# Optimization experiments

Measured on AMD Instinct MI355X. Metric: run time of the kernel, lower is better.

Reference implementation:

```python
import jax, jax.numpy as jnp
import numpy as np


def setup_inputs() -> dict:
    key = jax.random.key(0)
    k1, k2, k3, k4 = jax.random.split(key, 4)
    B, n, f, k = 32768, 512, 30, 40
    X = jax.random.normal(k1, (B, n), dtype=jnp.float32)
    w1 = jax.random.normal(k2, (n, 1), dtype=jnp.float32) * 0.01
    b = jnp.zeros((1,), dtype=jnp.float32)
    v = jax.random.normal(k3, (n, f, k), dtype=jnp.float32) * 0.01
    feature2field = jax.random.randint(k4, (n,), 0, f, dtype=jnp.int32)
    return {"X": X, "w1": w1, "b": b, "v": v, "feature2field": feature2field}


def reference(X, w1, b, v, feature2field):
    # linear terms: [B]
    linear = (X @ w1).reshape(-1) + b[0]
    n = v.shape[0]
    # A[i, j] = v[i, feature2field[j]]  -> [n, n, k]
    A = v[:, feature2field, :]
    # pair coefficient C[i, j] = sum_k v[i, field[j], k] * v[j, field[i], k]
    C = jnp.einsum('ijk,jik->ij', A, A)
    # strict upper triangle matches the i<j loop in the original
    Cm = C * jnp.triu(jnp.ones((n, n), dtype=C.dtype), k=1)
    # interaction[b] = sum_{i<j} C[i,j] * X[b,i] * X[b,j]
    inter = jnp.einsum('bi,ij,bj->b', X, Cm, X)
    logits = linear + inter
    return jax.nn.sigmoid(logits)
```

## Files before the change

kernel.cpp:

```cpp
#include <hip/hip_runtime.h>
#include <hip/hip_bf16.h>
#include <math.h>


#define N_FEAT 512
#define FK 1200
#define KDIM 40
#define B_ROWS 32768
#define BM 64
#define BK 64

typedef __attribute__((ext_vector_type(8))) short short8;
typedef __attribute__((ext_vector_type(4))) float f32x4;

__device__ __forceinline__ unsigned short bf16_rne(float f) {
    union { float f; unsigned int u; } c; c.f = f;
    unsigned int u = c.u;
    u += 0x7fffu + ((u >> 16) & 1u);
    return (unsigned short)(u >> 16);
}

__device__ __forceinline__ float bf16_to_f(unsigned short h) {
    union { unsigned int u; float f; } c;
    c.u = ((unsigned int)h) << 16;
    return c.f;
}

__device__ __forceinline__ void async_copy16(const void* g, void* l) {
    __builtin_amdgcn_global_load_lds(
        (const __attribute__((address_space(1))) void*)g,
        (__attribute__((address_space(3))) void*)l,
        16, 0, 0);
}

__global__ __launch_bounds__(256) void build_w16(const float* __restrict__ v,
                                                 const int* __restrict__ f2f,
                                                 unsigned short* __restrict__ W16) {
    const int j = blockIdx.x * 256 + threadIdx.x;
    const int i = blockIdx.y;
    const int fi = f2f[i];
    const int fj = f2f[j];
    const float4* a = (const float4*)(v + (size_t)i * FK + (size_t)fj * KDIM);
    const float4* c = (const float4*)(v + (size_t)j * FK + (size_t)fi * KDIM);
    float acc = 0.f;
#pragma unroll
    for (int q = 0; q < KDIM / 4; ++q) {
        float4 av = a[q], cv = c[q];
        acc = fmaf(av.x, cv.x, acc);
        acc = fmaf(av.y, cv.y, acc);
        acc = fmaf(av.z, cv.z, acc);
        acc = fmaf(av.w, cv.w, acc);
    }
    W16[(size_t)i * N_FEAT + j] = (i == j) ? (unsigned short)0 : bf16_rne(0.5f * acc);
}

__global__ __launch_bounds__(256, 2) void ffm_fused(const float* __restrict__ X,
                                                    const unsigned short* __restrict__ W16,
                                                    const float* __restrict__ w1,
                                                    const float* __restrict__ bvec,
                                                    float* __restrict__ out) {
    __shared__ __align__(16) unsigned short As[BM * N_FEAT];
    __shared__ __align__(16) unsigned short Bs[128 * BK];
    float* part = (float*)Bs;

    const int tid  = threadIdx.x;
    const int lane = tid & 63;
    const int wave = tid >> 6;
    const int wm = wave & 1;
    const int wn = wave >> 1;
    const int quad = lane >> 4;
    const int l16  = lane & 15;

    const size_t row0 = (size_t)blockIdx.x * BM;

    {
        const float4* X4 = (const float4*)(X + row0 * N_FEAT);
        for (int u = 0; u < 16; ++u) {
            const int g  = u * 256 + tid;
            const int r  = g >> 6;
            const int cc = g & 63;
            float4 f0 = X4[r * 128 + cc * 2];
            float4 f1 = X4[r * 128 + cc * 2 + 1];
            union { unsigned short us[8]; short8 v; } pk;
            pk.us[0] = bf16_rne(f0.x);
            pk.us[1] = bf16_rne(f0.y);
            pk.us[2] = bf16_rne(f0.z);
            pk.us[3] = bf16_rne(f0.w);
            pk.us[4] = bf16_rne(f1.x);
            pk.us[5] = bf16_rne(f1.y);
            pk.us[6] = bf16_rne(f1.z);
            pk.us[7] = bf16_rne(f1.w);
            *(short8*)(As + r * N_FEAT + ((cc ^ (r & 7)) << 3)) = pk.v;
        }
    }

    const int srow = lane >> 3;
    const int scol = (((lane & 7) ^ srow) << 3);
    const int aswz = l16 & 7;

    float rs[2][4];
#pragma unroll
    for (int mi = 0; mi < 2; ++mi)
#pragma unroll
        for (int reg = 0; reg < 4; ++reg) rs[mi][reg] = 0.f;

    for (int cb = 0; cb < 4; ++cb) {
        const int col0 = cb * 128;

        f32x4 acc[2][4];
#pragma unroll
        for (int mi = 0; mi < 2; ++mi)
#pragma unroll
            for (int ni = 0; ni < 4; ++ni)
                acc[mi][ni] = (f32x4){0.f, 0.f, 0.f, 0.f};

        for (int k0 = 0; k0 < N_FEAT; k0 += BK) {
            __syncthreads();
#pragma unroll
            for (int c = 0; c < 4; ++c) {
                const int chunk = wave * 4 + c;
                const int r = chunk * 8 + srow;
                async_copy16(W16 + (size_t)(col0 + r) * N_FEAT + k0 + scol,
                             Bs + chunk * 512);
            }
            __syncthreads();

#pragma unroll
            for (int kk = 0; kk < 2; ++kk) {
                short8 a[2], b[4];
                const int kc = (k0 >> 3) + kk * 4 + quad;
#pragma unroll
                for (int mi = 0; mi < 2; ++mi) {
                    const int ar = wm * 32 + mi * 16 + l16;
                    a[mi] = *(const short8*)(As + ar * N_FEAT + ((kc ^ aswz) << 3));
                }
                const int swc = ((kk * 4 + quad) ^ aswz) << 3;
#pragma unroll
                for (int ni = 0; ni < 4; ++ni) {
                    const int br = wn * 64 + ni * 16 + l16;
                    b[ni] = *(const short8*)(Bs + br * BK + swc);
                }
#pragma unroll
                for (int mi = 0; mi < 2; ++mi)
#pragma unroll
                    for (int ni = 0; ni < 4; ++ni)
                        acc[mi][ni] = __builtin_amdgcn_mfma_f32_16x16x32_bf16(
                            a[mi], b[ni], acc[mi][ni], 0, 0, 0);
            }
        }

        float w1v[4];
#pragma unroll
        for (int ni = 0; ni < 4; ++ni)
            w1v[ni] = w1[col0 + wn * 64 + ni * 16 + l16];
#pragma unroll
        for (int mi = 0; mi < 2; ++mi) {
#pragma unroll
            for (int ni = 0; ni < 4; ++ni) {
                const int gc = col0 + wn * 64 + ni * 16 + l16;
#pragma unroll
                for (int reg = 0; reg < 4; ++reg) {
                    const int row = wm * 32 + mi * 16 + quad * 4 + reg;
                    const int adr = row * N_FEAT + ((((gc >> 3) ^ (row & 7)) << 3) | (gc & 7));
                    const float xf = bf16_to_f(As[adr]);
                    rs[mi][reg] = fmaf(xf, acc[mi][ni][reg] + w1v[ni], rs[mi][reg]);
                }
            }
        }
    }

    __syncthreads();

#pragma unroll
    for (int mi = 0; mi < 2; ++mi)
#pragma unroll
        for (int reg = 0; reg < 4; ++reg) {
            float r = rs[mi][reg];
#pragma unroll
            for (int off = 1; off < 16; off <<= 1)
                r += __shfl_xor(r, off, 16);
            if (l16 == 0)
                part[wn * BM + wm * 32 + mi * 16 + quad * 4 + reg] = r;
        }
    __syncthreads();

    if (tid < BM) {
        const float t = part[tid] + part[BM + tid] + bvec[0];
        out[row0 + tid] = 1.0f / (1.0f + expf(-t));
    }
}

extern "C" void kernel_launch(void* const* d_in, const int* in_sizes, int n_in,
                              void* d_out, int out_size, void* d_ws, size_t ws_size,
                              hipStream_t stream) {
    const float* X   = (const float*)d_in[0];
    const float* w1  = (const float*)d_in[1];
    const float* b   = (const float*)d_in[2];
    const float* v   = (const float*)d_in[3];
    const int*   f2f = (const int*)d_in[4];
    float* out = (float*)d_out;

    unsigned short* W16 = (unsigned short*)d_ws;

    build_w16<<<dim3(2, N_FEAT), 256, 0, stream>>>(v, f2f, W16);
    ffm_fused<<<B_ROWS / BM, 256, 0, stream>>>(X, W16, w1, b, out);
}
```

Before: 126.3 us.

## Pipeline W tile loads with 4-stage LDS ring and compute linear term in fp32

Replaces the synchronous load-then-compute loop over W tiles with a flattened 32-step schedule that prefetches two tiles ahead into a 4-buffer LDS ring. It uses vmcnt waits plus one barrier per step instead of two __syncthreads. The linear term is now computed in fp32 during X staging via a wave reduction, rather than being added to the accumulators in the epilogue. LDS use grows to about 128KB and launch bounds drop to one block per CU, so occupancy falls in exchange for overlapping global-to-LDS copies with MFMA work.

```diff
diff --git a/kernel.cpp b/kernel.cpp
--- a/kernel.cpp
+++ b/kernel.cpp
@@ -8,7 +8,6 @@
 #define KDIM 40
 #define B_ROWS 32768
 #define BM 64
-#define BK 64
 
 typedef __attribute__((ext_vector_type(8))) short short8;
 typedef __attribute__((ext_vector_type(4))) float f32x4;
@@ -54,14 +53,15 @@
     W16[(size_t)i * N_FEAT + j] = (i == j) ? (unsigned short)0 : bf16_rne(0.5f * acc);
 }
 
-__global__ __launch_bounds__(256, 2) void ffm_fused(const float* __restrict__ X,
+__global__ __launch_bounds__(256, 1) void ffm_fused(const float* __restrict__ X,
                                                     const unsigned short* __restrict__ W16,
                                                     const float* __restrict__ w1,
                                                     const float* __restrict__ bvec,
                                                     float* __restrict__ out) {
     __shared__ __align__(16) unsigned short As[BM * N_FEAT];
-    __shared__ __align__(16) unsigned short Bs[128 * BK];
-    float* part = (float*)Bs;
+    __shared__ __align__(16) unsigned short Bs[4][128 * 64];
+    __shared__ float part[2][BM];
+    __shared__ float plin[BM];
 
     const int tid  = threadIdx.x;
     const int lane = tid & 63;
@@ -70,15 +70,18 @@
     const int wn = wave >> 1;
     const int quad = lane >> 4;
     const int l16  = lane & 15;
+    const int aswz = l16 & 7;
 
     const size_t row0 = (size_t)blockIdx.x * BM;
 
     {
         const float4* X4 = (const float4*)(X + row0 * N_FEAT);
+        const float4 wA = ((const float4*)w1)[lane * 2];
+        const float4 wB = ((const float4*)w1)[lane * 2 + 1];
+#pragma unroll
         for (int u = 0; u < 16; ++u) {
-            const int g  = u * 256 + tid;
-            const int r  = g >> 6;
-            const int cc = g & 63;
+            const int r  = u * 4 + wave;
+            const int cc = lane;
             float4 f0 = X4[r * 128 + cc * 2];
             float4 f1 = X4[r * 128 + cc * 2 + 1];
             union { unsigned short us[8]; short8 v; } pk;
@@ -91,85 +94,108 @@
             pk.us[6] = bf16_rne(f1.z);
             pk.us[7] = bf16_rne(f1.w);
             *(short8*)(As + r * N_FEAT + ((cc ^ (r & 7)) << 3)) = pk.v;
-        }
-    }
+            float lp = f0.x * wA.x + f0.y * wA.y + f0.z * wA.z + f0.w * wA.w
+                     + f1.x * wB.x + f1.y * wB.y + f1.z * wB.z + f1.w * wB.w;
+#pragma unroll
+            for (int off = 1; off < 64; off <<= 1)
+                lp += __shfl_xor(lp, off, 64);
+            if (lane == 0) plin[r] = lp;
+        }
+    }
+    __syncthreads();
 
     const int srow = lane >> 3;
-    const int scol = (((lane & 7) ^ srow) << 3);
-    const int aswz = l16 & 7;
+    const int scol = ((lane & 7) ^ srow) << 3;
 
     float rs[2][4];
+    f32x4 acc[2][4];
 #pragma unroll
     for (int mi = 0; mi < 2; ++mi)
 #pragma unroll
+        for (int ni = 0; ni < 4; ++ni) {
+            acc[mi][ni] = (f32x4){0.f, 0.f, 0.f, 0.f};
+            if (ni < 4) {}
+        }
+#pragma unroll
+    for (int mi = 0; mi < 2; ++mi)
+#pragma unroll
         for (int reg = 0; reg < 4; ++reg) rs[mi][reg] = 0.f;
 
-    for (int cb = 0; cb < 4; ++cb) {
-        const int col0 = cb * 128;
-
-        f32x4 acc[2][4];
-#pragma unroll
-        for (int mi = 0; mi < 2; ++mi)
-#pragma unroll
-            for (int ni = 0; ni < 4; ++ni)
-                acc[mi][ni] = (f32x4){0.f, 0.f, 0.f, 0.f};
-
-        for (int k0 = 0; k0 < N_FEAT; k0 += BK) {
-            __syncthreads();
-#pragma unroll
-            for (int c = 0; c < 4; ++c) {
-                const int chunk = wave * 4 + c;
-                const int r = chunk * 8 + srow;
-                async_copy16(W16 + (size_t)(col0 + r) * N_FEAT + k0 + scol,
-                             Bs + chunk * 512);
+    auto stage = [&](int t) {
+        unsigned short* buf = &Bs[t & 3][0];
+        const int col0 = (t >> 3) * 128;
+        const int k0   = (t & 7) * 64;
+#pragma unroll
+        for (int c = 0; c < 4; ++c) {
+            const int chunk = wave * 4 + c;
+            const int r = chunk * 8 + srow;
+            async_copy16(W16 + (size_t)(col0 + r) * N_FEAT + k0 + scol,
+                         buf + chunk * 512);
+        }
+    };
+
+    auto compute = [&](int t) {
+        const unsigned short* buf = &Bs[t & 3][0];
+        const int k0 = (t & 7) * 64;
+#pragma unroll
+        for (int kk = 0; kk < 2; ++kk) {
+            short8 a[2], b[4];
+            const int kc = (k0 >> 3) + kk * 4 + quad;
+#pragma unroll
+            for (int mi = 0; mi < 2; ++mi) {
+                const int ar = wm * 32 + mi * 16 + l16;
+                a[mi] = *(const short8*)(As + ar * N_FEAT + ((kc ^ aswz) << 3));
             }
-            __syncthreads();
-
-#pragma unroll
-            for (int kk = 0; kk < 2; ++kk) {
-                short8 a[2], b[4];
-                const int kc = (k0 >> 3) + kk * 4 + quad;
-#pragma unroll
-                for (int mi = 0; mi < 2; ++mi) {
-                    const int ar = wm * 32 + mi * 16 + l16;
-                    a[mi] = *(const short8*)(As + ar * N_FEAT + ((kc ^ aswz) << 3));
-                }
-                const int swc = ((kk * 4 + quad) ^ aswz) << 3;
-#pragma unroll
-                for (int ni = 0; ni < 4; ++ni) {
-                    const int br = wn * 64 + ni * 16 + l16;
-                    b[ni] = *(const short8*)(Bs + br * BK + swc);
-                }
-#pragma unroll
-                for (int mi = 0; mi < 2; ++mi)
-#pragma unroll
-                    for (int ni = 0; ni < 4; ++ni)
-                        acc[mi][ni] = __builtin_amdgcn_mfma_f32_16x16x32_bf16(
-                            a[mi], b[ni], acc[mi][ni], 0, 0, 0);
+            const int swc = ((kk * 4 + quad) ^ aswz) << 3;
+#pragma unroll
+            for (int ni = 0; ni < 4; ++ni) {
+                const int br = wn * 64 + ni * 16 + l16;
+                b[ni] = *(const short8*)(buf + br * 64 + swc);
             }
-        }
-
-        float w1v[4];
-#pragma unroll
-        for (int ni = 0; ni < 4; ++ni)
-            w1v[ni] = w1[col0 + wn * 64 + ni * 16 + l16];
+#pragma unroll
+            for (int mi = 0; mi < 2; ++mi)
+#pragma unroll
+                for (int ni = 0; ni < 4; ++ni)
+                    acc[mi][ni] = __builtin_amdgcn_mfma_f32_16x16x32_bf16(
+                        a[mi], b[ni], acc[mi][ni], 0, 0, 0);
+        }
+    };
+
+    auto epilogue = [&](int cb) {
 #pragma unroll
         for (int mi = 0; mi < 2; ++mi) {
 #pragma unroll
             for (int ni = 0; ni < 4; ++ni) {
-                const int gc = col0 + wn * 64 + ni * 16 + l16;
+                const int gc = cb * 128 + wn * 64 + ni * 16 + l16;
 #pragma unroll
                 for (int reg = 0; reg < 4; ++reg) {
                     const int row = wm * 32 + mi * 16 + quad * 4 + reg;
-                    const int adr = row * N_FEAT + ((((gc >> 3) ^ (row & 7)) << 3) | (gc & 7));
-                    const float xf = bf16_to_f(As[adr]);
-                    rs[mi][reg] = fmaf(xf, acc[mi][ni][reg] + w1v[ni], rs[mi][reg]);
+                    const int adr = row * N_FEAT +
+                                    ((((gc >> 3) ^ (row & 7)) << 3) | (gc & 7));
+                    rs[mi][reg] = fmaf(bf16_to_f(As[adr]), acc[mi][ni][reg],
+                                       rs[mi][reg]);
                 }
+                acc[mi][ni] = (f32x4){0.f, 0.f, 0.f, 0.f};
             }
         }
-    }
-
-    __syncthreads();
+    };
+
+    stage(0);
+    stage(1);
+    for (int s = 0; s < 30; ++s) {
+        stage(s + 2);
+        asm volatile("s_waitcnt vmcnt(8)" ::: "memory");
+        __builtin_amdgcn_s_barrier();
+        compute(s);
+        if ((s & 7) == 7) epilogue(s >> 3);
+    }
+    asm volatile("s_waitcnt vmcnt(4)" ::: "memory");
+    __builtin_amdgcn_s_barrier();
+    compute(30);
+    asm volatile("s_waitcnt vmcnt(0)" ::: "memory");
+    __builtin_amdgcn_s_barrier();
+    compute(31);
+    epilogue(3);
 
 #pragma unroll
     for (int mi = 0; mi < 2; ++mi)
@@ -180,12 +206,12 @@
             for (int off = 1; off < 16; off <<= 1)
                 r += __shfl_xor(r, off, 16);
             if (l16 == 0)
-                part[wn * BM + wm * 32 + mi * 16 + quad * 4 + reg] = r;
+                part[wn][wm * 32 + mi * 16 + quad * 4 + reg] = r;
         }
     __syncthreads();
 
     if (tid < BM) {
-        const float t = part[tid] + part[BM + tid] + bvec[0];
+        const float t = part[0][tid] + part[1][tid] + plin[tid] + bvec[0];
         out[row0 + tid] = 1.0f / (1.0f + expf(-t));
     }
 }
```

Measured after the change: 153.6 us. +21.6%, slower.
